# Kernel optimization log

Hardware: AMD Instinct MI355X
Metric: run time of the kernel (lower is better)

Reference implementation:

```python
import jax, jax.numpy as jnp
import numpy as np

H = 4          # n_hidden (forced by Linear(4, 4880) and GRU(4, n_hidden) feeding from embedding)
L = 2          # n_layers
DICT = 4880    # dict_size == fc1 out_features
MAXLEN = 6     # vec_out has exactly 6 time slots
B = 2048
T = 914        # max_point_len


def gru_cell(x, h, Wih, Whh, bih, bhh):
    """PyTorch GRU cell: gates ordered (r, z, n)."""
    gi = x @ Wih.T + bih            # (B, 3H)
    gh = h @ Whh.T + bhh            # (B, 3H)
    ir, iz, inn = jnp.split(gi, 3, axis=-1)
    hr, hz, hn = jnp.split(gh, 3, axis=-1)
    r = jax.nn.sigmoid(ir + hr)
    z = jax.nn.sigmoid(iz + hz)
    n = jnp.tanh(inn + r * hn)
    return (1.0 - z) * n + z * h


def setup_inputs() -> dict:
    key = jax.random.key(0)
    ks = jax.random.split(key, 24)
    s = jnp.float32(0.2)
    d = {}
    d["x"] = jax.random.normal(ks[0], (B, T, 2), dtype=jnp.float32)
    # encoder GRU: layer0 in=2, layer1 in=H
    d["enc_Wih0"] = jax.random.normal(ks[1], (3 * H, 2), dtype=jnp.float32) * s
    d["enc_Whh0"] = jax.random.normal(ks[2], (3 * H, H), dtype=jnp.float32) * s
    d["enc_bih0"] = jax.random.normal(ks[3], (3 * H,), dtype=jnp.float32) * s
    d["enc_bhh0"] = jax.random.normal(ks[4], (3 * H,), dtype=jnp.float32) * s
    d["enc_Wih1"] = jax.random.normal(ks[5], (3 * H, H), dtype=jnp.float32) * s
    d["enc_Whh1"] = jax.random.normal(ks[6], (3 * H, H), dtype=jnp.float32) * s
    d["enc_bih1"] = jax.random.normal(ks[7], (3 * H,), dtype=jnp.float32) * s
    d["enc_bhh1"] = jax.random.normal(ks[8], (3 * H,), dtype=jnp.float32) * s
    # decoder GRU: in=4 == H for both layers
    d["dec_Wih0"] = jax.random.normal(ks[9], (3 * H, H), dtype=jnp.float32) * s
    d["dec_Whh0"] = jax.random.normal(ks[10], (3 * H, H), dtype=jnp.float32) * s
    d["dec_bih0"] = jax.random.normal(ks[11], (3 * H,), dtype=jnp.float32) * s
    d["dec_bhh0"] = jax.random.normal(ks[12], (3 * H,), dtype=jnp.float32) * s
    d["dec_Wih1"] = jax.random.normal(ks[13], (3 * H, H), dtype=jnp.float32) * s
    d["dec_Whh1"] = jax.random.normal(ks[14], (3 * H, H), dtype=jnp.float32) * s
    d["dec_bih1"] = jax.random.normal(ks[15], (3 * H,), dtype=jnp.float32) * s
    d["dec_bhh1"] = jax.random.normal(ks[16], (3 * H,), dtype=jnp.float32) * s
    d["emb"] = jax.random.normal(ks[17], (DICT, H), dtype=jnp.float32) * s
    d["fc_W"] = jax.random.normal(ks[18], (DICT, H), dtype=jnp.float32) * s
    d["fc_b"] = jax.random.normal(ks[19], (DICT,), dtype=jnp.float32) * s
    d["fc1_W"] = jax.random.normal(ks[20], (DICT, H), dtype=jnp.float32) * s
    d["fc1_b"] = jax.random.normal(ks[21], (DICT,), dtype=jnp.float32) * s
    return d


def reference(x, enc_Wih0, enc_Whh0, enc_bih0, enc_bhh0,
              enc_Wih1, enc_Whh1, enc_bih1, enc_bhh1,
              dec_Wih0, dec_Whh0, dec_bih0, dec_bhh0,
              dec_Wih1, dec_Whh1, dec_bih1, dec_bhh1,
              emb, fc_W, fc_b, fc1_W, fc1_b):
    batch = x.shape[0]
    # ---- encoder: 2-layer GRU over time ----
    inp = jnp.transpose(x, (1, 0, 2))          # (T, B, 2)
    h0 = jnp.zeros((batch, H), dtype=x.dtype)
    finals = []
    for (Wih, Whh, bih, bhh) in ((enc_Wih0, enc_Whh0, enc_bih0, enc_bhh0),
                                 (enc_Wih1, enc_Whh1, enc_bih1, enc_bhh1)):
        def step(h, xt, Wih=Wih, Whh=Whh, bih=bih, bhh=bhh):
            hn = gru_cell(xt, h, Wih, Whh, bih, bhh)
            return hn, hn
        hT, outs = jax.lax.scan(step, h0, inp)
        inp = outs                              # (T, B, H)
        finals.append(hT)
    h_enc = jnp.stack(finals)                   # (L, B, H)
    _enc_out = h_enc[-1] @ fc_W.T + fc_b        # computed by original encoder(); unused downstream
    tok0 = jnp.zeros((batch,), dtype=jnp.int32)
    def dec_step(carry, _):
        tok, h = carry                          # tok (B,), h (L, B, H)
        e = emb[tok]                            # (B, H)
        h0n = gru_cell(e, h[0], dec_Wih0, dec_Whh0, dec_bih0, dec_bhh0)
        h1n = gru_cell(h0n, h[1], dec_Wih1, dec_Whh1, dec_bih1, dec_bhh1)
        logits = h1n @ fc1_W.T + fc1_b          # (B, DICT)
        nxt = jnp.argmax(logits, axis=-1).astype(jnp.int32)
        return (nxt, jnp.stack([h0n, h1n])), logits
    (_, _), logits_seq = jax.lax.scan(dec_step, (tok0, h_enc), None, length=MAXLEN)
    vec_out = jnp.transpose(logits_seq, (1, 0, 2))   # (B, MAXLEN, DICT)
    return vec_out, h_enc
```

## Files before the change

kernel.cpp:

```cpp
#include <hip/hip_runtime.h>
#include <stdint.h>

#define TT     914
#define BB     2048
#define DICTN  4880
#define MAXLEN 6
#define HENC_OFF ((size_t)BB * MAXLEN * DICTN)

__device__ __forceinline__ float bf2f(uint16_t u) {
    union { uint32_t i; float f; } v; v.i = ((uint32_t)u) << 16; return v.f;
}
__device__ __forceinline__ float bf2f_lo(uint32_t d) {
    union { uint32_t i; float f; } v; v.i = d << 16; return v.f;
}
__device__ __forceinline__ float bf2f_hi(uint32_t d) {
    union { uint32_t i; float f; } v; v.i = d & 0xFFFF0000u; return v.f;
}
__device__ __forceinline__ uint16_t f2bf(float f) {
    union { uint32_t i; float f; } v; v.f = f;
    uint32_t i = v.i;
    uint32_t r = i + 0x7FFFu + ((i >> 16) & 1u);
    return (uint16_t)(r >> 16);
}

__device__ __forceinline__ float fsigmoid(float x) {
    return __builtin_amdgcn_rcpf(1.0f + __expf(-x));
}
__device__ __forceinline__ float ftanh(float x) {
    return fmaf(-2.0f, __builtin_amdgcn_rcpf(1.0f + __expf(2.0f * x)), 1.0f);
}

#define DOT4(W, a0, a1, a2, a3, b) \
    fmaf((W)[0], (a0), fmaf((W)[1], (a1), fmaf((W)[2], (a2), fmaf((W)[3], (a3), (b)))))

#define DPP_XOR1 0xB1
#define DPP_XOR2 0x4E
#define DPP_XOR3 0x1B

template<int CTRL>
__device__ __forceinline__ int dpp_i(int v) {
    return __builtin_amdgcn_mov_dpp(v, CTRL, 0xF, 0xF, true);
}
template<int CTRL>
__device__ __forceinline__ float dpp_f(float v) {
    return __int_as_float(dpp_i<CTRL>(__float_as_int(v)));
}

typedef unsigned int uvec2 __attribute__((ext_vector_type(2)));

__device__ __forceinline__ float from_lo(float v) {
    uvec2 r = __builtin_amdgcn_permlane32_swap(__float_as_uint(v),
                                               __float_as_uint(v), false, false);
    return __uint_as_float(r[0]);
}
__device__ __forceinline__ float xhalf_f(float v, bool hi) {
    uvec2 r = __builtin_amdgcn_permlane32_swap(__float_as_uint(v),
                                               __float_as_uint(v), false, false);
    return __uint_as_float(hi ? r[0] : r[1]);
}
__device__ __forceinline__ int xhalf_i(int v, bool hi) {
    uvec2 r = __builtin_amdgcn_permlane32_swap((unsigned int)v,
                                               (unsigned int)v, false, false);
    return (int)(hi ? r[0] : r[1]);
}

template<bool F32> struct XVT { using T = uint2;  };
template<>         struct XVT<true> { using T = float4; };

template<bool F32>
__device__ __forceinline__ float ldw(const void* p, int i) {
    if constexpr (F32) return ((const float*)p)[i];
    else               return bf2f(((const uint16_t*)p)[i]);
}

template<bool F32>
__device__ __forceinline__ void t2s_body(
    const void* __restrict__ x,
    const void* __restrict__ eWih0, const void* __restrict__ eWhh0,
    const void* __restrict__ ebih0, const void* __restrict__ ebhh0,
    const void* __restrict__ eWih1, const void* __restrict__ eWhh1,
    const void* __restrict__ ebih1, const void* __restrict__ ebhh1,
    const void* __restrict__ dWih0, const void* __restrict__ dWhh0,
    const void* __restrict__ dbih0, const void* __restrict__ dbhh0,
    const void* __restrict__ dWih1, const void* __restrict__ dWhh1,
    const void* __restrict__ dbih1, const void* __restrict__ dbhh1,
    const void* __restrict__ emb,
    const void* __restrict__ fc1W, const void* __restrict__ fc1b,
    void* __restrict__ out)
{
    const int  lane  = threadIdx.x;
    const int  j     = lane & 3;
    const int  bgrp  = (lane >> 2) & 7;
    const bool is_l1 = (lane >= 32);
    const int  b     = blockIdx.x * 8 + bgrp;

    float p0, p1, p2, p3, q0, q1, q2, q3;

    {
        const void* Wih = is_l1 ? eWih1 : eWih0;
        const void* Whh = is_l1 ? eWhh1 : eWhh0;
        const void* bip = is_l1 ? ebih1 : ebih0;
        const void* bhp = is_l1 ? ebhh1 : ebhh0;

        float Wi[3][4], Wh[3][4], bi[3], bh[3];
        #pragma unroll
        for (int g = 0; g < 3; ++g) {
            const int row = g * 4 + j;
            bi[g] = ldw<F32>(bip, row);
            bh[g] = ldw<F32>(bhp, row);
            #pragma unroll
            for (int m = 0; m < 4; ++m)
                Wh[g][m] = ldw<F32>(Whh, row * 4 + (j ^ m));
            if (is_l1) {
                #pragma unroll
                for (int m = 0; m < 4; ++m)
                    Wi[g][m] = ldw<F32>(Wih, row * 4 + (j ^ m));
            } else {
                Wi[g][0] = ldw<F32>(Wih, row * 2 + 0);
                Wi[g][1] = ldw<F32>(Wih, row * 2 + 1);
                Wi[g][2] = 0.0f; Wi[g][3] = 0.0f;
            }
        }

        using XV = typename XVT<F32>::T;
        const XV* __restrict__ xp =
            (const XV*)((const char*)x + (size_t)b * (TT * 2) * (F32 ? 4 : 2));

        float hv0 = 0.f, hv1 = 0.f, hv2 = 0.f, hv3 = 0.f;
        float xf0 = 0.f, xf1 = 0.f, xf2 = 0.f, xf3 = 0.f;

        XV bufA_lo = xp[0], bufA_hi = xp[1];
        XV bufB_lo = xp[2], bufB_hi = xp[3];
        const XV xt = xp[456];

        for (int c = 0; c < 229; ++c) {
            XV lo = bufA_lo, hi = bufA_hi;
            bufA_lo = bufB_lo; bufA_hi = bufB_hi;
            const int ci = min(c + 2, 227);
            bufB_lo = xp[2 * ci];
            bufB_hi = xp[2 * ci + 1];

            if (c == 228) lo = xt;

            #pragma unroll
            for (int s = 0; s < 4; ++s) {
                const int it = c * 4 + s;
                float x0, x1;
                if constexpr (F32) {
                    const float4 v = (s < 2) ? lo : hi;
                    x0 = (s & 1) ? v.z : v.x;
                    x1 = (s & 1) ? v.w : v.y;
                } else {
                    const uint32_t w = (s < 2) ? ((s & 1) ? lo.y : lo.x)
                                               : ((s & 1) ? hi.y : hi.x);
                    x0 = bf2f_lo(w); x1 = bf2f_hi(w);
                }

                const float in0 = is_l1 ? xf0 : x0;
                const float in1 = is_l1 ? xf1 : x1;
                const float in2 = is_l1 ? xf2 : 0.0f;
                const float in3 = is_l1 ? xf3 : 0.0f;

                const float gr = DOT4(Wi[0], in0, in1, in2, in3, bi[0]);
                const float gz = DOT4(Wi[1], in0, in1, in2, in3, bi[1]);
                const float gn = DOT4(Wi[2], in0, in1, in2, in3, bi[2]);
                const float hr = DOT4(Wh[0], hv0, hv1, hv2, hv3, bh[0]);
                const float hz = DOT4(Wh[1], hv0, hv1, hv2, hv3, bh[1]);
                const float hn = DOT4(Wh[2], hv0, hv1, hv2, hv3, bh[2]);

                const float r = fsigmoid(gr + hr);
                const float z = fsigmoid(gz + hz);
                const float n = ftanh(fmaf(r, hn, gn));
                const float hnew = fmaf(z, hv0 - n, n);

                const bool act = is_l1 ? (it >= 1 && it < 915) : (it < 914);
                const float hj = act ? hnew : hv0;

                hv0 = hj;
                hv1 = dpp_f<DPP_XOR1>(hj);
                hv2 = dpp_f<DPP_XOR2>(hj);
                hv3 = dpp_f<DPP_XOR3>(hj);
                xf0 = from_lo(hj);
                xf1 = dpp_f<DPP_XOR1>(xf0);
                xf2 = dpp_f<DPP_XOR2>(xf0);
                xf3 = dpp_f<DPP_XOR3>(xf0);
            }
        }

        const size_t hidx = HENC_OFF + ((size_t)(is_l1 ? 1 : 0) * BB + b) * 4 + j;
        if constexpr (F32) ((float*)out)[hidx] = hv0;
        else               ((uint16_t*)out)[hidx] = f2bf(hv0);

        const float o0 = xhalf_f(hv0, is_l1);
        const float o1 = xhalf_f(hv1, is_l1);
        const float o2 = xhalf_f(hv2, is_l1);
        const float o3 = xhalf_f(hv3, is_l1);
        p0 = is_l1 ? o0 : hv0;  p1 = is_l1 ? o1 : hv1;
        p2 = is_l1 ? o2 : hv2;  p3 = is_l1 ? o3 : hv3;
        q0 = is_l1 ? hv0 : o0;  q1 = is_l1 ? hv1 : o1;
        q2 = is_l1 ? hv2 : o2;  q3 = is_l1 ? hv3 : o3;
    }

    float Wi0[3][4], Wh0[3][4], bi0[3], bh0[3];
    float Wi1[3][4], Wh1[3][4], bi1[3], bh1[3];
    #pragma unroll
    for (int g = 0; g < 3; ++g) {
        const int row = g * 4 + j;
        bi0[g] = ldw<F32>(dbih0, row);  bh0[g] = ldw<F32>(dbhh0, row);
        bi1[g] = ldw<F32>(dbih1, row);  bh1[g] = ldw<F32>(dbhh1, row);
        #pragma unroll
        for (int m = 0; m < 4; ++m) {
            Wi0[g][m] = ldw<F32>(dWih0, row * 4 + m);
            Wh0[g][m] = ldw<F32>(dWhh0, row * 4 + (j ^ m));
            Wi1[g][m] = ldw<F32>(dWih1, row * 4 + (j ^ m));
            Wh1[g][m] = ldw<F32>(dWhh1, row * 4 + (j ^ m));
        }
    }

    const int sub2 = j | (is_l1 ? 4 : 0);

    int tok = 0;
    for (int st = 0; st < MAXLEN; ++st) {
        float e0, e1, e2, e3;
        if constexpr (F32) {
            const float4 ev = *(const float4*)((const float*)emb + (size_t)tok * 4);
            e0 = ev.x; e1 = ev.y; e2 = ev.z; e3 = ev.w;
        } else {
            const uint2 ev = *(const uint2*)((const uint16_t*)emb + (size_t)tok * 4);
            e0 = bf2f_lo(ev.x); e1 = bf2f_hi(ev.x);
            e2 = bf2f_lo(ev.y); e3 = bf2f_hi(ev.y);
        }

        {
            const float gr = DOT4(Wi0[0], e0, e1, e2, e3, bi0[0]);
            const float gz = DOT4(Wi0[1], e0, e1, e2, e3, bi0[1]);
            const float gn = DOT4(Wi0[2], e0, e1, e2, e3, bi0[2]);
            const float hr = DOT4(Wh0[0], p0, p1, p2, p3, bh0[0]);
            const float hz = DOT4(Wh0[1], p0, p1, p2, p3, bh0[1]);
            const float hn = DOT4(Wh0[2], p0, p1, p2, p3, bh0[2]);
            const float r = fsigmoid(gr + hr);
            const float z = fsigmoid(gz + hz);
            const float n = ftanh(fmaf(r, hn, gn));
            const float hnew = fmaf(z, p0 - n, n);
            p0 = hnew;
            p1 = dpp_f<DPP_XOR1>(hnew);
            p2 = dpp_f<DPP_XOR2>(hnew);
            p3 = dpp_f<DPP_XOR3>(hnew);
        }
        {
            const float gr = DOT4(Wi1[0], p0, p1, p2, p3, bi1[0]);
            const float gz = DOT4(Wi1[1], p0, p1, p2, p3, bi1[1]);
            const float gn = DOT4(Wi1[2], p0, p1, p2, p3, bi1[2]);
            const float hr = DOT4(Wh1[0], q0, q1, q2, q3, bh1[0]);
            const float hz = DOT4(Wh1[1], q0, q1, q2, q3, bh1[1]);
            const float hn = DOT4(Wh1[2], q0, q1, q2, q3, bh1[2]);
            const float r = fsigmoid(gr + hr);
            const float z = fsigmoid(gz + hz);
            const float n = ftanh(fmaf(r, hn, gn));
            const float hnew = fmaf(z, q0 - n, n);
            q0 = hnew;
            q1 = dpp_f<DPP_XOR1>(hnew);
            q2 = dpp_f<DPP_XOR2>(hnew);
            q3 = dpp_f<DPP_XOR3>(hnew);
        }

        const bool jb0 = (j & 1) != 0, jb1 = (j & 2) != 0;
        const float s0 = jb0 ? q1 : q0, s1 = jb0 ? q0 : q1;
        const float s2 = jb0 ? q3 : q2, s3 = jb0 ? q2 : q3;
        const float a0 = jb1 ? s2 : s0, a1 = jb1 ? s3 : s1;
        const float a2 = jb1 ? s0 : s2, a3 = jb1 ? s1 : s3;

        const size_t off = ((size_t)b * MAXLEN + st) * DICTN;
        float best = -3.4e38f;
        int   bidx = 0;

        for (int db = sub2; db < DICTN / 8; db += 8) {
            const int d0 = db * 8;
            float l[8];
            if constexpr (F32) {
                const float4* wr = (const float4*)((const float*)fc1W + (size_t)d0 * 4);
                const float4 bv0 = *(const float4*)((const float*)fc1b + d0);
                const float4 bv1 = *(const float4*)((const float*)fc1b + d0 + 4);
                const float bb[8] = { bv0.x, bv0.y, bv0.z, bv0.w,
                                      bv1.x, bv1.y, bv1.z, bv1.w };
                #pragma unroll
                for (int i = 0; i < 8; ++i) {
                    const float4 w = wr[i];
                    l[i] = fmaf(a0, w.x, fmaf(a1, w.y, fmaf(a2, w.z, fmaf(a3, w.w, bb[i]))));
                }
                float* op = (float*)out + off + d0;
                *(float4*)(op)     = float4{ l[0], l[1], l[2], l[3] };
                *(float4*)(op + 4) = float4{ l[4], l[5], l[6], l[7] };
            } else {
                const uint4* wp = (const uint4*)((const uint16_t*)fc1W + (size_t)d0 * 4);
                const uint4 w0 = wp[0], w1 = wp[1], w2 = wp[2], w3 = wp[3];
                const uint4 bv = *(const uint4*)((const uint16_t*)fc1b + d0);
                const uint32_t wa[16] = { w0.x, w0.y, w0.z, w0.w,
                                          w1.x, w1.y, w1.z, w1.w,
                                          w2.x, w2.y, w2.z, w2.w,
                                          w3.x, w3.y, w3.z, w3.w };
                const uint32_t ba[4] = { bv.x, bv.y, bv.z, bv.w };
                #pragma unroll
                for (int i = 0; i < 8; ++i) {
                    const uint32_t da  = wa[2 * i];
                    const uint32_t db2 = wa[2 * i + 1];
                    float acc = (i & 1) ? bf2f_hi(ba[i >> 1]) : bf2f_lo(ba[i >> 1]);
                    acc = fmaf(a0, bf2f_lo(da), acc);
                    acc = fmaf(a1, bf2f_hi(da), acc);
                    acc = fmaf(a2, bf2f_lo(db2), acc);
                    acc = fmaf(a3, bf2f_hi(db2), acc);
                    l[i] = acc;
                }
                uint4 ov;
                ov.x = (uint32_t)f2bf(l[0]) | ((uint32_t)f2bf(l[1]) << 16);
                ov.y = (uint32_t)f2bf(l[2]) | ((uint32_t)f2bf(l[3]) << 16);
                ov.z = (uint32_t)f2bf(l[4]) | ((uint32_t)f2bf(l[5]) << 16);
                ov.w = (uint32_t)f2bf(l[6]) | ((uint32_t)f2bf(l[7]) << 16);
                *(uint4*)((uint16_t*)out + off + d0) = ov;
            }
            #pragma unroll
            for (int i = 0; i < 8; ++i) {
                if (l[i] > best) { best = l[i]; bidx = d0 + i; }
            }
        }

        {
            const float ov = dpp_f<DPP_XOR1>(best);
            const int   oi = dpp_i<DPP_XOR1>(bidx);
            if (ov > best || (ov == best && oi < bidx)) { best = ov; bidx = oi; }
        }
        {
            const float ov = dpp_f<DPP_XOR2>(best);
            const int   oi = dpp_i<DPP_XOR2>(bidx);
            if (ov > best || (ov == best && oi < bidx)) { best = ov; bidx = oi; }
        }
        {
            const float ov = xhalf_f(best, is_l1);
            const int   oi = xhalf_i(bidx, is_l1);
            if (ov > best || (ov == best && oi < bidx)) { best = ov; bidx = oi; }
        }
        tok = ((unsigned)bidx < (unsigned)DICTN) ? bidx : 0;
    }
}

__global__ __launch_bounds__(64, 1) void t2s_fused(
    const void* __restrict__ x,
    const void* __restrict__ eWih0, const void* __restrict__ eWhh0,
    const void* __restrict__ ebih0, const void* __restrict__ ebhh0,
    const void* __restrict__ eWih1, const void* __restrict__ eWhh1,
    const void* __restrict__ ebih1, const void* __restrict__ ebhh1,
    const void* __restrict__ dWih0, const void* __restrict__ dWhh0,
    const void* __restrict__ dbih0, const void* __restrict__ dbhh0,
    const void* __restrict__ dWih1, const void* __restrict__ dWhh1,
    const void* __restrict__ dbih1, const void* __restrict__ dbhh1,
    const void* __restrict__ emb,
    const void* __restrict__ fc1W, const void* __restrict__ fc1b,
    void* __restrict__ out)
{
    const uint16_t* pw = (const uint16_t*)eWhh0;
    int cnt = 0;
    #pragma unroll
    for (int k = 0; k < 12; ++k) {
        const float av = fabsf(bf2f(pw[2 * k]));
        if (av >= 0.000244140625f && av <= 8.0f) ++cnt;
    }
    const bool is_bf16 = (cnt >= 7);

    if (is_bf16)
        t2s_body<false>(x, eWih0, eWhh0, ebih0, ebhh0, eWih1, eWhh1, ebih1, ebhh1,
                        dWih0, dWhh0, dbih0, dbhh0, dWih1, dWhh1, dbih1, dbhh1,
                        emb, fc1W, fc1b, out);
    else
        t2s_body<true>(x, eWih0, eWhh0, ebih0, ebhh0, eWih1, eWhh1, ebih1, ebhh1,
                       dWih0, dWhh0, dbih0, dbhh0, dWih1, dWhh1, dbih1, dbhh1,
                       emb, fc1W, fc1b, out);
}

extern "C" void kernel_launch(void* const* d_in, const int* in_sizes, int n_in,
                              void* d_out, int out_size, void* d_ws, size_t ws_size,
                              hipStream_t stream)
{
    (void)d_ws; (void)ws_size; (void)in_sizes; (void)n_in; (void)out_size;

    t2s_fused<<<BB / 8, 64, 0, stream>>>(
        d_in[0],
        d_in[1], d_in[2], d_in[3], d_in[4],
        d_in[5], d_in[6], d_in[7], d_in[8],
        d_in[9], d_in[10], d_in[11], d_in[12],
        d_in[13], d_in[14], d_in[15], d_in[16],
        d_in[17],
        d_in[20], d_in[21],
        d_out);
}
```

Measured before the change: 717.8 us.

## Prescale GRU weights for exp2 activations and precompute input gates off the recurrence path

Folds the sigmoid and tanh scale constants (-log2e and 2*log2e) into the GRU weights and biases at load time, so each activation becomes a single exp2 plus reciprocal and tanh is rewritten as a sigmoid. The input-gate dot products for the next timestep are computed right after the state update. The recurrent FMA chain then starts from the precomputed input-gate value, which shortens the serial dependency chain per step. The first and last timesteps are peeled out of the loop, removing the per-step active-mask select. Numerics change slightly from the reordered FMAs and the exp2 rewrite.

```diff
diff --git a/kernel.cpp b/kernel.cpp
--- a/kernel.cpp
+++ b/kernel.cpp
@@ -23,15 +23,12 @@
     return (uint16_t)(r >> 16);
 }
 
-__device__ __forceinline__ float fsigmoid(float x) {
-    return __builtin_amdgcn_rcpf(1.0f + __expf(-x));
-}
-__device__ __forceinline__ float ftanh(float x) {
-    return fmaf(-2.0f, __builtin_amdgcn_rcpf(1.0f + __expf(2.0f * x)), 1.0f);
-}
-
-#define DOT4(W, a0, a1, a2, a3, b) \
-    fmaf((W)[0], (a0), fmaf((W)[1], (a1), fmaf((W)[2], (a2), fmaf((W)[3], (a3), (b)))))
+__device__ __forceinline__ float sig2(float x) {
+    return __builtin_amdgcn_rcpf(1.0f + __builtin_amdgcn_exp2f(x));
+}
+
+#define TDOT(W, a0, a1, a2, a3, b) \
+    fmaf((W)[3], (a3), fmaf((W)[2], (a2), fmaf((W)[1], (a1), fmaf((W)[0], (a0), (b)))))
 
 #define DPP_XOR1 0xB1
 #define DPP_XOR2 0x4E
@@ -72,6 +69,9 @@
     if constexpr (F32) return ((const float*)p)[i];
     else               return bf2f(((const uint16_t*)p)[i]);
 }
+
+#define C_SIG  (-1.44269504088896340736f)
+#define C_TANH ( 2.88539008177792681472f)
 
 template<bool F32>
 __device__ __forceinline__ void t2s_body(
@@ -94,6 +94,8 @@
     const bool is_l1 = (lane >= 32);
     const int  b     = blockIdx.x * 8 + bgrp;
 
+    const float cs[3] = { C_SIG, C_SIG, C_TANH };
+
     float p0, p1, p2, p3, q0, q1, q2, q3;
 
     {
@@ -106,21 +108,25 @@
         #pragma unroll
         for (int g = 0; g < 3; ++g) {
             const int row = g * 4 + j;
-            bi[g] = ldw<F32>(bip, row);
-            bh[g] = ldw<F32>(bhp, row);
+            bi[g] = cs[g] * ldw<F32>(bip, row);
+            bh[g] = cs[g] * ldw<F32>(bhp, row);
             #pragma unroll
             for (int m = 0; m < 4; ++m)
-                Wh[g][m] = ldw<F32>(Whh, row * 4 + (j ^ m));
+                Wh[g][m] = cs[g] * ldw<F32>(Whh, row * 4 + (j ^ m));
             if (is_l1) {
                 #pragma unroll
                 for (int m = 0; m < 4; ++m)
-                    Wi[g][m] = ldw<F32>(Wih, row * 4 + (j ^ m));
+                    Wi[g][m] = cs[g] * ldw<F32>(Wih, row * 4 + (j ^ m));
             } else {
-                Wi[g][0] = ldw<F32>(Wih, row * 2 + 0);
-                Wi[g][1] = ldw<F32>(Wih, row * 2 + 1);
+                Wi[g][0] = cs[g] * ldw<F32>(Wih, row * 2 + 0);
+                Wi[g][1] = cs[g] * ldw<F32>(Wih, row * 2 + 1);
                 Wi[g][2] = 0.0f; Wi[g][3] = 0.0f;
             }
         }
+        const float bsum0 = bi[0] + bh[0];
+        const float bsum1 = bi[1] + bh[1];
+        const float bin   = bi[2];
+        const float bhn   = bh[2];
 
         using XV = typename XVT<F32>::T;
         const XV* __restrict__ xp =
@@ -128,63 +134,98 @@
 
         float hv0 = 0.f, hv1 = 0.f, hv2 = 0.f, hv3 = 0.f;
         float xf0 = 0.f, xf1 = 0.f, xf2 = 0.f, xf3 = 0.f;
+        float grf = 0.f, gzf = 0.f, gnf = 0.f;
 
         XV bufA_lo = xp[0], bufA_hi = xp[1];
         XV bufB_lo = xp[2], bufB_hi = xp[3];
         const XV xt = xp[456];
 
-        for (int c = 0; c < 229; ++c) {
+        auto GIN = [&](float nx0, float nx1) {
+            const float i0 = is_l1 ? xf0 : nx0;
+            const float i1 = is_l1 ? xf1 : nx1;
+            const float i2 = is_l1 ? xf2 : 0.0f;
+            const float i3 = is_l1 ? xf3 : 0.0f;
+            grf = TDOT(Wi[0], i0, i1, i2, i3, bsum0);
+            gzf = TDOT(Wi[1], i0, i1, i2, i3, bsum1);
+            gnf = TDOT(Wi[2], i0, i1, i2, i3, bin);
+        };
+        auto CORE = [&]() -> float {
+            const float hr = TDOT(Wh[0], hv0, hv1, hv2, hv3, grf);
+            const float hz = TDOT(Wh[1], hv0, hv1, hv2, hv3, gzf);
+            const float hn = TDOT(Wh[2], hv0, hv1, hv2, hv3, bhn);
+            const float r  = sig2(hr);
+            const float z  = sig2(hz);
+            const float u  = sig2(fmaf(r, hn, gnf));
+            return fmaf(z, fmaf(2.0f, u, hv0 - 1.0f), fmaf(-2.0f, u, 1.0f));
+        };
+        auto UPD = [&](float hj) {
+            hv0 = hj;
+            hv1 = dpp_f<DPP_XOR1>(hj);
+            hv2 = dpp_f<DPP_XOR2>(hj);
+            hv3 = dpp_f<DPP_XOR3>(hj);
+            xf0 = from_lo(hj);
+            xf1 = dpp_f<DPP_XOR1>(xf0);
+            xf2 = dpp_f<DPP_XOR2>(xf0);
+            xf3 = dpp_f<DPP_XOR3>(xf0);
+        };
+        auto NEXTX = [&](int s, XV lo, XV hi, float& nx0, float& nx1) {
+            if constexpr (F32) {
+                if      (s == 0) { nx0 = lo.z;      nx1 = lo.w; }
+                else if (s == 1) { nx0 = hi.x;      nx1 = hi.y; }
+                else if (s == 2) { nx0 = hi.z;      nx1 = hi.w; }
+                else             { nx0 = bufA_lo.x; nx1 = bufA_lo.y; }
+            } else {
+                uint32_t w;
+                if      (s == 0) w = lo.y;
+                else if (s == 1) w = hi.x;
+                else if (s == 2) w = hi.y;
+                else             w = bufA_lo.x;
+                nx0 = bf2f_lo(w); nx1 = bf2f_hi(w);
+            }
+        };
+
+        if constexpr (F32) GIN(bufA_lo.x, bufA_lo.y);
+        else               GIN(bf2f_lo(bufA_lo.x), bf2f_hi(bufA_lo.x));
+
+        {
+            XV lo = bufA_lo, hi = bufA_hi;
+            bufA_lo = bufB_lo; bufA_hi = bufB_hi;
+            bufB_lo = xp[4];   bufB_hi = xp[5];
+            #pragma unroll
+            for (int s = 0; s < 4; ++s) {
+                const float hnew = CORE();
+                const float hj = (s == 0) ? (is_l1 ? 0.0f : hnew) : hnew;
+                UPD(hj);
+                float nx0, nx1; NEXTX(s, lo, hi, nx0, nx1);
+                GIN(nx0, nx1);
+            }
+        }
+
+        for (int c = 1; c < 228; ++c) {
             XV lo = bufA_lo, hi = bufA_hi;
             bufA_lo = bufB_lo; bufA_hi = bufB_hi;
             const int ci = min(c + 2, 227);
             bufB_lo = xp[2 * ci];
             bufB_hi = xp[2 * ci + 1];
-
-            if (c == 228) lo = xt;
-
             #pragma unroll
             for (int s = 0; s < 4; ++s) {
-                const int it = c * 4 + s;
-                float x0, x1;
-                if constexpr (F32) {
-                    const float4 v = (s < 2) ? lo : hi;
-                    x0 = (s & 1) ? v.z : v.x;
-                    x1 = (s & 1) ? v.w : v.y;
-                } else {
-                    const uint32_t w = (s < 2) ? ((s & 1) ? lo.y : lo.x)
-                                               : ((s & 1) ? hi.y : hi.x);
-                    x0 = bf2f_lo(w); x1 = bf2f_hi(w);
-                }
-
-                const float in0 = is_l1 ? xf0 : x0;
-                const float in1 = is_l1 ? xf1 : x1;
-                const float in2 = is_l1 ? xf2 : 0.0f;
-                const float in3 = is_l1 ? xf3 : 0.0f;
-
-                const float gr = DOT4(Wi[0], in0, in1, in2, in3, bi[0]);
-                const float gz = DOT4(Wi[1], in0, in1, in2, in3, bi[1]);
-                const float gn = DOT4(Wi[2], in0, in1, in2, in3, bi[2]);
-                const float hr = DOT4(Wh[0], hv0, hv1, hv2, hv3, bh[0]);
-                const float hz = DOT4(Wh[1], hv0, hv1, hv2, hv3, bh[1]);
-                const float hn = DOT4(Wh[2], hv0, hv1, hv2, hv3, bh[2]);
-
-                const float r = fsigmoid(gr + hr);
-                const float z = fsigmoid(gz + hz);
-                const float n = ftanh(fmaf(r, hn, gn));
-                const float hnew = fmaf(z, hv0 - n, n);
-
-                const bool act = is_l1 ? (it >= 1 && it < 915) : (it < 914);
-                const float hj = act ? hnew : hv0;
-
-                hv0 = hj;
-                hv1 = dpp_f<DPP_XOR1>(hj);
-                hv2 = dpp_f<DPP_XOR2>(hj);
-                hv3 = dpp_f<DPP_XOR3>(hj);
-                xf0 = from_lo(hj);
-                xf1 = dpp_f<DPP_XOR1>(xf0);
-                xf2 = dpp_f<DPP_XOR2>(xf0);
-                xf3 = dpp_f<DPP_XOR3>(xf0);
-            }
+                UPD(CORE());
+                float nx0, nx1; NEXTX(s, lo, hi, nx0, nx1);
+                GIN(nx0, nx1);
+            }
+        }
+
+        if constexpr (F32) GIN(xt.x, xt.y);
+        else               GIN(bf2f_lo(xt.x), bf2f_hi(xt.x));
+        UPD(CORE());
+        if constexpr (F32) GIN(xt.z, xt.w);
+        else               GIN(bf2f_lo(xt.y), bf2f_hi(xt.y));
+        UPD(CORE());
+        GIN(0.0f, 0.0f);
+        {
+            const float hnew = CORE();
+            const float hj = is_l1 ? hnew : hv0;
+            UPD(hj);
         }
 
         const size_t hidx = HENC_OFF + ((size_t)(is_l1 ? 1 : 0) * BB + b) * 4 + j;
@@ -206,16 +247,18 @@
     #pragma unroll
     for (int g = 0; g < 3; ++g) {
         const int row = g * 4 + j;
-        bi0[g] = ldw<F32>(dbih0, row);  bh0[g] = ldw<F32>(dbhh0, row);
-        bi1[g] = ldw<F32>(dbih1, row);  bh1[g] = ldw<F32>(dbhh1, row);
+        bi0[g] = cs[g] * ldw<F32>(dbih0, row);  bh0[g] = cs[g] * ldw<F32>(dbhh0, row);
+        bi1[g] = cs[g] * ldw<F32>(dbih1, row);  bh1[g] = cs[g] * ldw<F32>(dbhh1, row);
         #pragma unroll
         for (int m = 0; m < 4; ++m) {
-            Wi0[g][m] = ldw<F32>(dWih0, row * 4 + m);
-            Wh0[g][m] = ldw<F32>(dWhh0, row * 4 + (j ^ m));
-            Wi1[g][m] = ldw<F32>(dWih1, row * 4 + (j ^ m));
-            Wh1[g][m] = ldw<F32>(dWhh1, row * 4 + (j ^ m));
+            Wi0[g][m] = cs[g] * ldw<F32>(dWih0, row * 4 + m);
+            Wh0[g][m] = cs[g] * ldw<F32>(dWhh0, row * 4 + (j ^ m));
+            Wi1[g][m] = cs[g] * ldw<F32>(dWih1, row * 4 + (j ^ m));
+            Wh1[g][m] = cs[g] * ldw<F32>(dWhh1, row * 4 + (j ^ m));
         }
     }
+    const float bs0r = bi0[0] + bh0[0], bs0z = bi0[1] + bh0[1];
+    const float bs1r = bi1[0] + bh1[0], bs1z = bi1[1] + bh1[1];
 
     const int sub2 = j | (is_l1 ? 4 : 0);
 
@@ -232,32 +275,32 @@
         }
 
         {
-            const float gr = DOT4(Wi0[0], e0, e1, e2, e3, bi0[0]);
-            const float gz = DOT4(Wi0[1], e0, e1, e2, e3, bi0[1]);
-            const float gn = DOT4(Wi0[2], e0, e1, e2, e3, bi0[2]);
-            const float hr = DOT4(Wh0[0], p0, p1, p2, p3, bh0[0]);
-            const float hz = DOT4(Wh0[1], p0, p1, p2, p3, bh0[1]);
-            const float hn = DOT4(Wh0[2], p0, p1, p2, p3, bh0[2]);
-            const float r = fsigmoid(gr + hr);
-            const float z = fsigmoid(gz + hz);
-            const float n = ftanh(fmaf(r, hn, gn));
-            const float hnew = fmaf(z, p0 - n, n);
+            const float grf = TDOT(Wi0[0], e0, e1, e2, e3, bs0r);
+            const float gzf = TDOT(Wi0[1], e0, e1, e2, e3, bs0z);
+            const float gnf = TDOT(Wi0[2], e0, e1, e2, e3, bi0[2]);
+            const float hr  = TDOT(Wh0[0], p0, p1, p2, p3, grf);
+            const float hz  = TDOT(Wh0[1], p0, p1, p2, p3, gzf);
+            const float hn  = TDOT(Wh0[2], p0, p1, p2, p3, bh0[2]);
+            const float r   = sig2(hr);
+            const float z   = sig2(hz);
+            const float u   = sig2(fmaf(r, hn, gnf));
+            const float hnew = fmaf(z, fmaf(2.0f, u, p0 - 1.0f), fmaf(-2.0f, u, 1.0f));
             p0 = hnew;
             p1 = dpp_f<DPP_XOR1>(hnew);
             p2 = dpp_f<DPP_XOR2>(hnew);
             p3 = dpp_f<DPP_XOR3>(hnew);
         }
         {
-            const float gr = DOT4(Wi1[0], p0, p1, p2, p3, bi1[0]);
-            const float gz = DOT4(Wi1[1], p0, p1, p2, p3, bi1[1]);
-            const float gn = DOT4(Wi1[2], p0, p1, p2, p3, bi1[2]);
-            const float hr = DOT4(Wh1[0], q0, q1, q2, q3, bh1[0]);
-            const float hz = DOT4(Wh1[1], q0, q1, q2, q3, bh1[1]);
-            const float hn = DOT4(Wh1[2], q0, q1, q2, q3, bh1[2]);
-            const float r = fsigmoid(gr + hr);
-            const float z = fsigmoid(gz + hz);
-            const float n = ftanh(fmaf(r, hn, gn));
-            const float hnew = fmaf(z, q0 - n, n);
+            const float grf = TDOT(Wi1[0], p0, p1, p2, p3, bs1r);
+            const float gzf = TDOT(Wi1[1], p0, p1, p2, p3, bs1z);
+            const float gnf = TDOT(Wi1[2], p0, p1, p2, p3, bi1[2]);
+            const float hr  = TDOT(Wh1[0], q0, q1, q2, q3, grf);
+            const float hz  = TDOT(Wh1[1], q0, q1, q2, q3, gzf);
+            const float hn  = TDOT(Wh1[2], q0, q1, q2, q3, bh1[2]);
+            const float r   = sig2(hr);
+            const float z   = sig2(hz);
+            const float u   = sig2(fmaf(r, hn, gnf));
+            const float hnew = fmaf(z, fmaf(2.0f, u, q0 - 1.0f), fmaf(-2.0f, u, 1.0f));
             q0 = hnew;
             q1 = dpp_f<DPP_XOR1>(hnew);
             q2 = dpp_f<DPP_XOR2>(hnew);
```

After: 742.4 us. +3.4%, slower.
